# Kernel optimization log

Hardware: AMD Instinct MI355X
Metric: run time of the kernel (lower is better)

Reference implementation:

```python
import jax, jax.numpy as jnp
import numpy as np

N = 8192      # nodes
R = 3         # non-homo relations
E = 262144    # edges per relation (avg degree 32)
IN = 128      # input_dim
OUT = 64      # output_dim (= per-head dim hd)
HEAD = 4
D = OUT * HEAD  # 256, w_liner / d_liner output width


def setup_inputs() -> dict:
    key = jax.random.key(0)
    ks = jax.random.split(key, 16)
    s = 0.05  # weight scale (mimics uniform(-stdv, stdv) magnitude)
    return {
        "features": jax.random.normal(ks[0], (N, IN), jnp.float32),
        "labels_mat": jax.random.uniform(ks[1], (N, 2), jnp.float32),
        "bi_adj": jax.random.uniform(ks[2], (N, N), jnp.float32),
        "adj_mask": jax.random.uniform(ks[3], (N, N), jnp.float32),
        "Wd": jax.random.normal(ks[4], (IN, D), jnp.float32) * s,
        "bd": jax.random.normal(ks[5], (D,), jnp.float32) * s,
        "Wf": jax.random.normal(ks[6], (3 * D, 1), jnp.float32) * s,
        "bf": jax.random.normal(ks[7], (1,), jnp.float32) * s,
        "Ww": jax.random.normal(ks[8], (R, IN, D), jnp.float32) * s,
        "bw": jax.random.normal(ks[9], (R, D), jnp.float32) * s,
        "Wa": jax.random.normal(ks[10], (R, 2 * OUT), jnp.float32) * s,
        "ba": jax.random.normal(ks[11], (R,), jnp.float32) * s,
        "Wl": jax.random.normal(ks[12], (R * OUT, OUT), jnp.float32) * s,
        "bl": jax.random.normal(ks[13], (OUT,), jnp.float32) * s,
        "edges": jax.random.randint(ks[14], (R, 2, E), 0, N, jnp.int64),
    }


def reference(features, labels_mat, bi_adj, adj_mask, Wd, bd, Wf, bf,
              Ww, bw, Wa, ba, Wl, bl, edges):
    n = features.shape[0]
    r_count = edges.shape[0]
    d = Wd.shape[1]          # D = head * hd
    hd = d // HEAD

    # --- HeterophilyLearning (shared relation_aware), dropout is identity in eval.
    # score = tanh(f_liner(cat[src, dst, src-dst])); f_liner is linear, so
    # split Wf and precompute per-node contributions, then gather per edge.
    sproj = features @ Wd + bd                      # [N, D]
    w1, w2, w3 = Wf[:d, 0], Wf[d:2 * d, 0], Wf[2 * d:, 0]
    p_src = sproj @ (w1 + w3)                       # [N]
    p_dst = sproj @ (w2 - w3)                       # [N]

    hs = []
    for r in range(r_count):  # small fixed loop over relations
        src, dst = edges[r, 0], edges[r, 1]
        sign = jnp.tanh(p_src[src] + p_dst[dst] + bf[0])          # [E]
        h = (features @ Ww[r] + bw[r]).reshape(n, HEAD, hd)       # [N, H, hd]
        # atten(cat[sign*h_src, h_dst]) decomposed into src/dst node terms
        qsrc = jnp.einsum('nhd,d->nh', h, Wa[r, :hd])             # [N, H]
        qdst = jnp.einsum('nhd,d->nh', h, Wa[r, hd:])             # [N, H]
        alpha = jax.nn.leaky_relu(sign[:, None] * qsrc[src] + qdst[dst] + ba[r])  # [E, H]
        # ragged softmax over incoming edges of each dst node
        m = jax.ops.segment_max(alpha, dst, num_segments=n)
        m = jnp.where(jnp.isfinite(m), m, 0.0)
        ew = jnp.exp(alpha - m[dst])
        denom = jax.ops.segment_sum(ew, dst, num_segments=n)
        attn = ew / denom[dst]                                    # [E, H]
        sf = sign[:, None, None] * h[src]                         # [E, H, hd]
        out = jax.ops.segment_sum(attn[:, :, None] * sf, dst, num_segments=n)  # [N, H, hd]
        hs.append(out.sum(axis=1))  # if_sum=True in Aggregation -> sum heads -> [N, hd]

    hcat = jnp.concatenate(hs, axis=1)              # [N, R*hd]
    h_out = hcat @ Wl + bl                          # dropout identity in eval

    # --- Label propagation (last relation's Homo, as in the original loop)
    T = bi_adj * adj_mask
    T = T / jnp.maximum(jnp.abs(T).sum(axis=1, keepdims=True), 1e-12)  # F.normalize p=1
    y_hat = T @ labels_mat
    return h_out, y_hat
```

## Files before the change

kernel.cpp:

```cpp
#include <hip/hip_runtime.h>
#include <hip/hip_bf16.h>
#include <math.h>

constexpr int kN    = 8192;
constexpr int kR    = 3;
constexpr int kE    = 262144;
constexpr int kIn   = 128;
constexpr int kOut  = 64;
constexpr int kHead = 4;
constexpr int kD    = 256;

__global__ __launch_bounds__(256) void k_node_pre(
    const float* __restrict__ feat, const float* __restrict__ Wd,
    const float* __restrict__ bd,   const float* __restrict__ Wf,
    const float* __restrict__ Ww,   const float* __restrict__ bw,
    const float* __restrict__ Wa,
    float* __restrict__ p_src, float* __restrict__ p_dst,
    float* __restrict__ qsrc,  float* __restrict__ qdst,
    float* __restrict__ hbuf)
{
    const int n = blockIdx.x, t = threadIdx.x;
    __shared__ float f[kIn];
    __shared__ float2 red[256];

    if (t < kIn) f[t] = feat[n * kIn + t];
    __syncthreads();

    float sp = bd[t];
    #pragma unroll 8
    for (int k = 0; k < kIn; ++k) sp += f[k] * Wd[k * kD + t];

    const float w13 = Wf[t]        + Wf[2 * kD + t];
    const float w23 = Wf[kD + t]   - Wf[2 * kD + t];
    red[t] = make_float2(sp * w13, sp * w23);
    __syncthreads();
    for (int s = 128; s > 0; s >>= 1) {
        if (t < s) { red[t].x += red[t + s].x; red[t].y += red[t + s].y; }
        __syncthreads();
    }
    if (t == 0) { p_src[n] = red[0].x; p_dst[n] = red[0].y; }

    const int head = t >> 6, lane = t & 63;
    for (int r = 0; r < kR; ++r) {
        float hv = bw[r * kD + t];
        const float* W = Ww + (size_t)r * kIn * kD;
        #pragma unroll 8
        for (int k = 0; k < kIn; ++k) hv += f[k] * W[k * kD + t];
        hbuf[(size_t)r * kN * kD + (size_t)n * kD + t] = hv;

        float c1 = hv * Wa[r * 2 * kOut + lane];
        float c2 = hv * Wa[r * 2 * kOut + kOut + lane];
        for (int off = 32; off > 0; off >>= 1) {
            c1 += __shfl_down(c1, off);
            c2 += __shfl_down(c2, off);
        }
        if (lane == 0) {
            qsrc[(size_t)r * kN * kHead + n * kHead + head] = c1;
            qdst[(size_t)r * kN * kHead + n * kHead + head] = c2;
        }
    }
}

__global__ void k_hist(const int* __restrict__ dst, int* __restrict__ deg)
{
    int e = blockIdx.x * blockDim.x + threadIdx.x;
    if (e < kE) atomicAdd(&deg[dst[e]], 1);
}

__global__ __launch_bounds__(1024) void k_scan(
    const int* __restrict__ deg, int* __restrict__ rowstart)
{
    __shared__ int lds[1024];
    const int t = threadIdx.x;
    int v[8];
    int s = 0;
    #pragma unroll
    for (int k = 0; k < 8; ++k) v[k] = deg[t * 8 + k];
    #pragma unroll
    for (int k = 0; k < 8; ++k) { int tmp = s; s += v[k]; v[k] = tmp; }
    lds[t] = s;
    __syncthreads();
    for (int off = 1; off < 1024; off <<= 1) {
        int x = 0;
        if (t >= off) x = lds[t - off];
        __syncthreads();
        if (t >= off) lds[t] += x;
        __syncthreads();
    }
    const int pre = (t == 0) ? 0 : lds[t - 1];
    #pragma unroll
    for (int k = 0; k < 8; ++k) rowstart[t * 8 + k] = pre + v[k];
}

__global__ void k_scatter(
    const int* __restrict__ src_arr, const int* __restrict__ dst_arr,
    const float* __restrict__ p_src, const float* __restrict__ p_dst,
    const float* __restrict__ qsrc,  const float* __restrict__ qdst,
    const float* __restrict__ bf,    const float* __restrict__ ba, int r,
    const int* __restrict__ rowstart, int* __restrict__ cursor,
    int* __restrict__ srcs_s, float* __restrict__ sign_s,
    float4* __restrict__ alpha_s)
{
    int e = blockIdx.x * blockDim.x + threadIdx.x;
    if (e >= kE) return;
    const int s = src_arr[e], d = dst_arr[e];
    const float sg = tanhf(p_src[s] + p_dst[d] + bf[0]);
    const float bar = ba[r];
    float4 a;
    float* ap = &a.x;
    #pragma unroll
    for (int h = 0; h < kHead; ++h) {
        float x = sg * qsrc[s * kHead + h] + qdst[d * kHead + h] + bar;
        ap[h] = (x > 0.f) ? x : 0.01f * x;
    }
    const int pos = rowstart[d] + atomicAdd(&cursor[d], 1);
    srcs_s[pos] = s;
    sign_s[pos] = sg;
    alpha_s[pos] = a;
}

__global__ __launch_bounds__(256) void k_node_agg(
    const int* __restrict__ deg, const int* __restrict__ rowstart,
    const int* __restrict__ srcs_s, const float* __restrict__ sign_s,
    const float4* __restrict__ alpha_s,
    const float* __restrict__ hr,
    float* __restrict__ hcat, int r)
{
    const int n = blockIdx.x, t = threadIdx.x;
    const int dg = deg[n], start = rowstart[n];
    __shared__ float4 red4[256];
    __shared__ float lds[256];

    if (dg == 0) {
        if (t < kOut) hcat[(size_t)n * (kR * kOut) + r * kOut + t] = 0.f;
        return;
    }

    float4 mx = make_float4(-INFINITY, -INFINITY, -INFINITY, -INFINITY);
    for (int i = t; i < dg; i += 256) {
        float4 a = alpha_s[start + i];
        mx.x = fmaxf(mx.x, a.x); mx.y = fmaxf(mx.y, a.y);
        mx.z = fmaxf(mx.z, a.z); mx.w = fmaxf(mx.w, a.w);
    }
    red4[t] = mx;
    __syncthreads();
    for (int s = 128; s > 0; s >>= 1) {
        if (t < s) {
            float4 o = red4[t + s];
            red4[t].x = fmaxf(red4[t].x, o.x); red4[t].y = fmaxf(red4[t].y, o.y);
            red4[t].z = fmaxf(red4[t].z, o.z); red4[t].w = fmaxf(red4[t].w, o.w);
        }
        __syncthreads();
    }
    const float4 mm = red4[0];
    const int head = t >> 6;
    const float m_h = (head == 0) ? mm.x : (head == 1) ? mm.y : (head == 2) ? mm.z : mm.w;

    const float* af = (const float*)alpha_s;
    float acc = 0.f, dsum = 0.f;
    for (int i = 0; i < dg; ++i) {
        const int pos = start + i;
        const float sg = sign_s[pos];
        const float a  = af[(size_t)pos * 4 + head];
        const float ew = __expf(a - m_h);
        dsum += ew;
        const int s = srcs_s[pos];
        acc += ew * sg * hr[(size_t)s * kD + t];
    }
    lds[t] = acc / dsum;
    __syncthreads();
    if (t < kOut) {
        hcat[(size_t)n * (kR * kOut) + r * kOut + t] =
            lds[t] + lds[t + 64] + lds[t + 128] + lds[t + 192];
    }
}

__global__ __launch_bounds__(64) void k_hout(
    const float* __restrict__ hcat, const float* __restrict__ Wl,
    const float* __restrict__ bl, float* __restrict__ out)
{
    const int n = blockIdx.x, t = threadIdx.x;
    __shared__ float row[kR * kOut];
    for (int k = t; k < kR * kOut; k += 64) row[k] = hcat[(size_t)n * (kR * kOut) + k];
    __syncthreads();
    float acc = bl[t];
    #pragma unroll 8
    for (int k = 0; k < kR * kOut; ++k) acc += row[k] * Wl[k * kOut + t];
    out[(size_t)n * kOut + t] = acc;
}

__global__ __launch_bounds__(256) void k_yhat(
    const float* __restrict__ bi, const float* __restrict__ mask,
    const float* __restrict__ labels, float* __restrict__ out)
{
    const int n = blockIdx.x, t = threadIdx.x;
    const float4* b4 = (const float4*)(bi   + (size_t)n * kN);
    const float4* m4 = (const float4*)(mask + (size_t)n * kN);
    const float4* l4 = (const float4*)labels;
    float ss = 0.f, y0 = 0.f, y1 = 0.f;
    for (int j = t; j < kN / 4; j += 256) {
        const float4 b = b4[j], m = m4[j];
        const float4 la = l4[2 * j], lb = l4[2 * j + 1];
        const float t0 = b.x * m.x, t1 = b.y * m.y, t2 = b.z * m.z, t3 = b.w * m.w;
        ss += fabsf(t0) + fabsf(t1) + fabsf(t2) + fabsf(t3);
        y0 += t0 * la.x + t1 * la.z + t2 * lb.x + t3 * lb.z;
        y1 += t0 * la.y + t1 * la.w + t2 * lb.y + t3 * lb.w;
    }
    __shared__ float4 red[256];
    red[t] = make_float4(ss, y0, y1, 0.f);
    __syncthreads();
    for (int s = 128; s > 0; s >>= 1) {
        if (t < s) {
            red[t].x += red[t + s].x; red[t].y += red[t + s].y; red[t].z += red[t + s].z;
        }
        __syncthreads();
    }
    if (t == 0) {
        const float s = fmaxf(red[0].x, 1e-12f);
        out[(size_t)n * 2]     = red[0].y / s;
        out[(size_t)n * 2 + 1] = red[0].z / s;
    }
}

extern "C" void kernel_launch(void* const* d_in, const int* in_sizes, int n_in,
                              void* d_out, int out_size, void* d_ws, size_t ws_size,
                              hipStream_t stream)
{
    const float* feat   = (const float*)d_in[0];
    const float* labels = (const float*)d_in[1];
    const float* bi     = (const float*)d_in[2];
    const float* mask   = (const float*)d_in[3];
    const float* Wd     = (const float*)d_in[4];
    const float* bd     = (const float*)d_in[5];
    const float* Wf     = (const float*)d_in[6];
    const float* bf     = (const float*)d_in[7];
    const float* Ww     = (const float*)d_in[8];
    const float* bw     = (const float*)d_in[9];
    const float* Wa     = (const float*)d_in[10];
    const float* ba     = (const float*)d_in[11];
    const float* Wl     = (const float*)d_in[12];
    const float* bl     = (const float*)d_in[13];
    const int*   edges  = (const int*)d_in[14];
    float* out = (float*)d_out;

    float* w = (float*)d_ws;
    float* p_src  = w; w += kN;
    float* p_dst  = w; w += kN;
    float* qsrc   = w; w += (size_t)kR * kN * kHead;
    float* qdst   = w; w += (size_t)kR * kN * kHead;
    float* hbuf   = w; w += (size_t)kR * kN * kD;
    float* hcat   = w; w += (size_t)kN * kR * kOut;
    float* sign_s = w; w += kE;
    float* alpha_s= w; w += (size_t)kE * 4;
    int* srcs_s   = (int*)w; w += kE;
    int* deg      = (int*)w; w += kN;
    int* rowstart = (int*)w; w += kN;
    int* cursor   = (int*)w; w += kN;

    k_node_pre<<<kN, 256, 0, stream>>>(feat, Wd, bd, Wf, Ww, bw, Wa,
                                       p_src, p_dst, qsrc, qdst, hbuf);

    for (int r = 0; r < kR; ++r) {
        const int* src_arr = edges + (size_t)r * 2 * kE;
        const int* dst_arr = src_arr + kE;
        hipMemsetAsync(deg,    0, kN * sizeof(int), stream);
        hipMemsetAsync(cursor, 0, kN * sizeof(int), stream);
        k_hist<<<kE / 256, 256, 0, stream>>>(dst_arr, deg);
        k_scan<<<1, 1024, 0, stream>>>(deg, rowstart);
        k_scatter<<<kE / 256, 256, 0, stream>>>(
            src_arr, dst_arr, p_src, p_dst,
            qsrc + (size_t)r * kN * kHead, qdst + (size_t)r * kN * kHead,
            bf, ba, r, rowstart, cursor, srcs_s, sign_s, (float4*)alpha_s);
        k_node_agg<<<kN, 256, 0, stream>>>(
            deg, rowstart, srcs_s, sign_s, (const float4*)alpha_s,
            hbuf + (size_t)r * kN * kD, hcat, r);
    }

    k_hout<<<kN, 64, 0, stream>>>(hcat, Wl, bl, out);
    k_yhat<<<kN, 256, 0, stream>>>(bi, mask, labels, out + (size_t)kN * kOut);
}
```

Baseline: 989.2 us.

## Fold projection weights, batch node GEMM, merge relation launches, stage edges in LDS

Adds a prep kernel that folds Wd·Wf and Ww·Wa into small column vectors, so p_src/p_dst and qsrc/qdst become direct dot products with the features. The node pre-pass now computes 16 nodes per block to reuse each Ww load across nodes. The per-relation loop of hist/scan/scatter/agg is collapsed into single launches using a relation grid dimension. The aggregation kernel caches up to 128 edges' alpha/sign/src in LDS. This removes the redundant sproj GEMM and many small launches, at the cost of more workspace and a serial single-block prep kernel.

```diff
diff --git a/kernel.cpp b/kernel.cpp
--- a/kernel.cpp
+++ b/kernel.cpp
@@ -9,67 +9,133 @@
 constexpr int kOut  = 64;
 constexpr int kHead = 4;
 constexpr int kD    = 256;
+constexpr int NB    = 16;
+constexpr int kCols = 2 + 2 * kR * kHead;
+
+__global__ __launch_bounds__(256) void k_prep(
+    const float* __restrict__ Wd, const float* __restrict__ bd,
+    const float* __restrict__ Wf, const float* __restrict__ Ww,
+    const float* __restrict__ bw, const float* __restrict__ Wa,
+    float* __restrict__ V, float* __restrict__ C)
+{
+    const int t = threadIdx.x;
+    for (int task = t; task < kCols * kIn; task += 256) {
+        const int row = task >> 7;
+        const int k   = task & 127;
+        float s = 0.f;
+        if (row < 2) {
+            for (int c = 0; c < kD; ++c) {
+                const float w = (row == 0) ? (Wf[c] + Wf[2 * kD + c])
+                                           : (Wf[kD + c] - Wf[2 * kD + c]);
+                s += Wd[k * kD + c] * w;
+            }
+        } else {
+            const int idx = row - 2;
+            const int src = idx < kR * kHead;
+            const int rel = (src ? idx : idx - kR * kHead) >> 2;
+            const int h   = (src ? idx : idx - kR * kHead) & 3;
+            const float* wwk = Ww + ((size_t)rel * kIn + k) * kD + h * kOut;
+            const float* wa  = Wa + rel * 2 * kOut + (src ? 0 : kOut);
+            for (int d = 0; d < kOut; ++d) s += wwk[d] * wa[d];
+        }
+        V[row * kIn + k] = s;
+    }
+    if (t < kCols) {
+        const int row = t;
+        float s = 0.f;
+        if (row < 2) {
+            for (int c = 0; c < kD; ++c) {
+                const float w = (row == 0) ? (Wf[c] + Wf[2 * kD + c])
+                                           : (Wf[kD + c] - Wf[2 * kD + c]);
+                s += bd[c] * w;
+            }
+        } else {
+            const int idx = row - 2;
+            const int src = idx < kR * kHead;
+            const int rel = (src ? idx : idx - kR * kHead) >> 2;
+            const int h   = (src ? idx : idx - kR * kHead) & 3;
+            const float* bwr = bw + rel * kD + h * kOut;
+            const float* wa  = Wa + rel * 2 * kOut + (src ? 0 : kOut);
+            for (int d = 0; d < kOut; ++d) s += bwr[d] * wa[d];
+        }
+        C[row] = s;
+    }
+}
 
 __global__ __launch_bounds__(256) void k_node_pre(
-    const float* __restrict__ feat, const float* __restrict__ Wd,
-    const float* __restrict__ bd,   const float* __restrict__ Wf,
-    const float* __restrict__ Ww,   const float* __restrict__ bw,
-    const float* __restrict__ Wa,
-    float* __restrict__ p_src, float* __restrict__ p_dst,
-    float* __restrict__ qsrc,  float* __restrict__ qdst,
-    float* __restrict__ hbuf)
-{
-    const int n = blockIdx.x, t = threadIdx.x;
-    __shared__ float f[kIn];
-    __shared__ float2 red[256];
-
-    if (t < kIn) f[t] = feat[n * kIn + t];
-    __syncthreads();
-
-    float sp = bd[t];
-    #pragma unroll 8
-    for (int k = 0; k < kIn; ++k) sp += f[k] * Wd[k * kD + t];
-
-    const float w13 = Wf[t]        + Wf[2 * kD + t];
-    const float w23 = Wf[kD + t]   - Wf[2 * kD + t];
-    red[t] = make_float2(sp * w13, sp * w23);
-    __syncthreads();
-    for (int s = 128; s > 0; s >>= 1) {
-        if (t < s) { red[t].x += red[t + s].x; red[t].y += red[t + s].y; }
-        __syncthreads();
-    }
-    if (t == 0) { p_src[n] = red[0].x; p_dst[n] = red[0].y; }
-
-    const int head = t >> 6, lane = t & 63;
+    const float* __restrict__ feat, const float* __restrict__ Ww,
+    const float* __restrict__ bw,   const float* __restrict__ V,
+    const float* __restrict__ C,
+    float* __restrict__ hbuf, float* __restrict__ p_src, float* __restrict__ p_dst,
+    float* __restrict__ qsrc, float* __restrict__ qdst)
+{
+    const int nb = blockIdx.x * NB;
+    const int t  = threadIdx.x;
+    __shared__ float f[NB][kIn];
+
+    const float4* fg = (const float4*)(feat + (size_t)nb * kIn);
+    float4* fl = (float4*)f;
+    for (int i = t; i < NB * kIn / 4; i += 256) fl[i] = fg[i];
+    __syncthreads();
+
     for (int r = 0; r < kR; ++r) {
-        float hv = bw[r * kD + t];
         const float* W = Ww + (size_t)r * kIn * kD;
-        #pragma unroll 8
-        for (int k = 0; k < kIn; ++k) hv += f[k] * W[k * kD + t];
-        hbuf[(size_t)r * kN * kD + (size_t)n * kD + t] = hv;
-
-        float c1 = hv * Wa[r * 2 * kOut + lane];
-        float c2 = hv * Wa[r * 2 * kOut + kOut + lane];
-        for (int off = 32; off > 0; off >>= 1) {
-            c1 += __shfl_down(c1, off);
-            c2 += __shfl_down(c2, off);
-        }
-        if (lane == 0) {
-            qsrc[(size_t)r * kN * kHead + n * kHead + head] = c1;
-            qdst[(size_t)r * kN * kHead + n * kHead + head] = c2;
-        }
-    }
-}
-
-__global__ void k_hist(const int* __restrict__ dst, int* __restrict__ deg)
-{
-    int e = blockIdx.x * blockDim.x + threadIdx.x;
-    if (e < kE) atomicAdd(&deg[dst[e]], 1);
+        const float b = bw[r * kD + t];
+        float acc[NB];
+        #pragma unroll
+        for (int j = 0; j < NB; ++j) acc[j] = b;
+        for (int k4 = 0; k4 < kIn / 4; ++k4) {
+            const float w0 = W[(k4 * 4 + 0) * kD + t];
+            const float w1 = W[(k4 * 4 + 1) * kD + t];
+            const float w2 = W[(k4 * 4 + 2) * kD + t];
+            const float w3 = W[(k4 * 4 + 3) * kD + t];
+            #pragma unroll
+            for (int j = 0; j < NB; ++j) {
+                const float4 fv = *(const float4*)&f[j][k4 * 4];
+                acc[j] += fv.x * w0 + fv.y * w1 + fv.z * w2 + fv.w * w3;
+            }
+        }
+        float* hb = hbuf + ((size_t)r * kN + nb) * kD + t;
+        #pragma unroll
+        for (int j = 0; j < NB; ++j) hb[(size_t)j * kD] = acc[j];
+    }
+
+    for (int task = t; task < NB * kCols; task += 256) {
+        const int j = task / kCols, col = task % kCols;
+        const float* v = V + col * kIn;
+        float s = C[col];
+        for (int k4 = 0; k4 < kIn / 4; ++k4) {
+            const float4 fv = *(const float4*)&f[j][k4 * 4];
+            const float4 vv = *(const float4*)&v[k4 * 4];
+            s += fv.x * vv.x + fv.y * vv.y + fv.z * vv.z + fv.w * vv.w;
+        }
+        const int n = nb + j;
+        if (col == 0)      p_src[n] = s;
+        else if (col == 1) p_dst[n] = s;
+        else if (col < 2 + kR * kHead) {
+            const int idx = col - 2;
+            qsrc[((size_t)(idx >> 2) * kN + n) * kHead + (idx & 3)] = s;
+        } else {
+            const int idx = col - 2 - kR * kHead;
+            qdst[((size_t)(idx >> 2) * kN + n) * kHead + (idx & 3)] = s;
+        }
+    }
+}
+
+__global__ void k_hist(const int* __restrict__ edges, int* __restrict__ deg)
+{
+    const int r = blockIdx.y;
+    const int e = blockIdx.x * blockDim.x + threadIdx.x;
+    const int d = edges[(size_t)r * 2 * kE + kE + e];
+    atomicAdd(&deg[r * kN + d], 1);
 }
 
 __global__ __launch_bounds__(1024) void k_scan(
-    const int* __restrict__ deg, int* __restrict__ rowstart)
-{
+    const int* __restrict__ deg_all, int* __restrict__ rowstart_all)
+{
+    const int r = blockIdx.x;
+    const int* deg = deg_all + r * kN;
+    int* rowstart = rowstart_all + r * kN;
     __shared__ int lds[1024];
     const int t = threadIdx.x;
     int v[8];
@@ -93,43 +159,57 @@
 }
 
 __global__ void k_scatter(
-    const int* __restrict__ src_arr, const int* __restrict__ dst_arr,
+    const int* __restrict__ edges,
     const float* __restrict__ p_src, const float* __restrict__ p_dst,
-    const float* __restrict__ qsrc,  const float* __restrict__ qdst,
-    const float* __restrict__ bf,    const float* __restrict__ ba, int r,
+    const float* __restrict__ qsrc_all, const float* __restrict__ qdst_all,
+    const float* __restrict__ bf, const float* __restrict__ ba,
     const int* __restrict__ rowstart, int* __restrict__ cursor,
     int* __restrict__ srcs_s, float* __restrict__ sign_s,
     float4* __restrict__ alpha_s)
 {
-    int e = blockIdx.x * blockDim.x + threadIdx.x;
-    if (e >= kE) return;
-    const int s = src_arr[e], d = dst_arr[e];
+    const int r = blockIdx.y;
+    const int e = blockIdx.x * blockDim.x + threadIdx.x;
+    const int s = edges[(size_t)r * 2 * kE + e];
+    const int d = edges[(size_t)r * 2 * kE + kE + e];
     const float sg = tanhf(p_src[s] + p_dst[d] + bf[0]);
     const float bar = ba[r];
+    const float4 qs = *(const float4*)&qsrc_all[((size_t)r * kN + s) * kHead];
+    const float4 qd = *(const float4*)&qdst_all[((size_t)r * kN + d) * kHead];
     float4 a;
-    float* ap = &a.x;
-    #pragma unroll
-    for (int h = 0; h < kHead; ++h) {
-        float x = sg * qsrc[s * kHead + h] + qdst[d * kHead + h] + bar;
-        ap[h] = (x > 0.f) ? x : 0.01f * x;
-    }
-    const int pos = rowstart[d] + atomicAdd(&cursor[d], 1);
-    srcs_s[pos] = s;
-    sign_s[pos] = sg;
-    alpha_s[pos] = a;
+    a.x = sg * qs.x + qd.x + bar;
+    a.y = sg * qs.y + qd.y + bar;
+    a.z = sg * qs.z + qd.z + bar;
+    a.w = sg * qs.w + qd.w + bar;
+    a.x = (a.x > 0.f) ? a.x : 0.01f * a.x;
+    a.y = (a.y > 0.f) ? a.y : 0.01f * a.y;
+    a.z = (a.z > 0.f) ? a.z : 0.01f * a.z;
+    a.w = (a.w > 0.f) ? a.w : 0.01f * a.w;
+    const int pos = rowstart[r * kN + d] + atomicAdd(&cursor[r * kN + d], 1);
+    srcs_s[(size_t)r * kE + pos] = s;
+    sign_s[(size_t)r * kE + pos] = sg;
+    alpha_s[(size_t)r * kE + pos] = a;
 }
 
 __global__ __launch_bounds__(256) void k_node_agg(
     const int* __restrict__ deg, const int* __restrict__ rowstart,
-    const int* __restrict__ srcs_s, const float* __restrict__ sign_s,
-    const float4* __restrict__ alpha_s,
-    const float* __restrict__ hr,
-    float* __restrict__ hcat, int r)
-{
+    const int* __restrict__ srcs_all, const float* __restrict__ sign_all,
+    const float4* __restrict__ alpha_all, const float* __restrict__ hbuf,
+    float* __restrict__ hcat)
+{
+    const int r = blockIdx.y;
     const int n = blockIdx.x, t = threadIdx.x;
-    const int dg = deg[n], start = rowstart[n];
+    const int dg = deg[r * kN + n], start = rowstart[r * kN + n];
+    const float* hr = hbuf + (size_t)r * kN * kD;
+    const int* srcs = srcs_all + (size_t)r * kE;
+    const float* sgn = sign_all + (size_t)r * kE;
+    const float4* al = alpha_all + (size_t)r * kE;
+
+    constexpr int CAP = 128;
     __shared__ float4 red4[256];
-    __shared__ float lds[256];
+    __shared__ float4 s_al[CAP];
+    __shared__ float  s_sg[CAP];
+    __shared__ int    s_sr[CAP];
+    __shared__ float  lds[256];
 
     if (dg == 0) {
         if (t < kOut) hcat[(size_t)n * (kR * kOut) + r * kOut + t] = 0.f;
@@ -138,7 +218,12 @@
 
     float4 mx = make_float4(-INFINITY, -INFINITY, -INFINITY, -INFINITY);
     for (int i = t; i < dg; i += 256) {
-        float4 a = alpha_s[start + i];
+        const float4 a = al[start + i];
+        if (i < CAP) {
+            s_al[i] = a;
+            s_sg[i] = sgn[start + i];
+            s_sr[i] = srcs[start + i];
+        }
         mx.x = fmaxf(mx.x, a.x); mx.y = fmaxf(mx.y, a.y);
         mx.z = fmaxf(mx.z, a.z); mx.w = fmaxf(mx.w, a.w);
     }
@@ -146,7 +231,7 @@
     __syncthreads();
     for (int s = 128; s > 0; s >>= 1) {
         if (t < s) {
-            float4 o = red4[t + s];
+            const float4 o = red4[t + s];
             red4[t].x = fmaxf(red4[t].x, o.x); red4[t].y = fmaxf(red4[t].y, o.y);
             red4[t].z = fmaxf(red4[t].z, o.z); red4[t].w = fmaxf(red4[t].w, o.w);
         }
@@ -154,18 +239,23 @@
     }
     const float4 mm = red4[0];
     const int head = t >> 6;
-    const float m_h = (head == 0) ? mm.x : (head == 1) ? mm.y : (head == 2) ? mm.z : mm.w;
-
-    const float* af = (const float*)alpha_s;
+    const float m_h = (head == 0) ? mm.x : (head == 1) ? mm.y
+                    : (head == 2) ? mm.z : mm.w;
+
     float acc = 0.f, dsum = 0.f;
-    for (int i = 0; i < dg; ++i) {
-        const int pos = start + i;
-        const float sg = sign_s[pos];
-        const float a  = af[(size_t)pos * 4 + head];
+    const int m = (dg < CAP) ? dg : CAP;
+    for (int i = 0; i < m; ++i) {
+        const float a  = ((const float*)&s_al[i])[head];
         const float ew = __expf(a - m_h);
         dsum += ew;
-        const int s = srcs_s[pos];
-        acc += ew * sg * hr[(size_t)s * kD + t];
+        acc += ew * s_sg[i] * hr[(size_t)s_sr[i] * kD + t];
+    }
+    for (int i = CAP; i < dg; ++i) {
+        const int pos = start + i;
+        const float a  = ((const float*)&al[pos])[head];
+        const float ew = __expf(a - m_h);
+        dsum += ew;
+        acc += ew * sgn[pos] * hr[(size_t)srcs[pos] * kD + t];
     }
     lds[t] = acc / dsum;
     __syncthreads();
@@ -248,33 +338,29 @@
     float* p_dst  = w; w += kN;
     float* qsrc   = w; w += (size_t)kR * kN * kHead;
     float* qdst   = w; w += (size_t)kR * kN * kHead;
+    float* V      = w; w += kCols * kIn;
+    float* C      = w; w += 32;
     float* hbuf   = w; w += (size_t)kR * kN * kD;
     float* hcat   = w; w += (size_t)kN * kR * kOut;
-    float* sign_s = w; w += kE;
-    float* alpha_s= w; w += (size_t)kE * 4;
-    int* srcs_s   = (int*)w; w += kE;
-    int* deg      = (int*)w; w += kN;
-    int* rowstart = (int*)w; w += kN;
-    int* cursor   = (int*)w; w += kN;
-
-    k_node_pre<<<kN, 256, 0, stream>>>(feat, Wd, bd, Wf, Ww, bw, Wa,
-                                       p_src, p_dst, qsrc, qdst, hbuf);
-
-    for (int r = 0; r < kR; ++r) {
-        const int* src_arr = edges + (size_t)r * 2 * kE;
-        const int* dst_arr = src_arr + kE;
-        hipMemsetAsync(deg,    0, kN * sizeof(int), stream);
-        hipMemsetAsync(cursor, 0, kN * sizeof(int), stream);
-        k_hist<<<kE / 256, 256, 0, stream>>>(dst_arr, deg);
-        k_scan<<<1, 1024, 0, stream>>>(deg, rowstart);
-        k_scatter<<<kE / 256, 256, 0, stream>>>(
-            src_arr, dst_arr, p_src, p_dst,
-            qsrc + (size_t)r * kN * kHead, qdst + (size_t)r * kN * kHead,
-            bf, ba, r, rowstart, cursor, srcs_s, sign_s, (float4*)alpha_s);
-        k_node_agg<<<kN, 256, 0, stream>>>(
-            deg, rowstart, srcs_s, sign_s, (const float4*)alpha_s,
-            hbuf + (size_t)r * kN * kD, hcat, r);
-    }
+    float* sign_s = w; w += (size_t)kR * kE;
+    float* alpha_s= w; w += (size_t)kR * kE * 4;
+    int* srcs_s   = (int*)w; w += (size_t)kR * kE;
+    int* deg      = (int*)w; w += kR * kN;
+    int* cursor   = (int*)w; w += kR * kN;
+    int* rowstart = (int*)w; w += kR * kN;
+
+    k_prep<<<1, 256, 0, stream>>>(Wd, bd, Wf, Ww, bw, Wa, V, C);
+    k_node_pre<<<kN / NB, 256, 0, stream>>>(feat, Ww, bw, V, C,
+                                            hbuf, p_src, p_dst, qsrc, qdst);
+
+    hipMemsetAsync(deg, 0, 2 * kR * kN * sizeof(int), stream);
+    k_hist<<<dim3(kE / 256, kR), 256, 0, stream>>>(edges, deg);
+    k_scan<<<kR, 1024, 0, stream>>>(deg, rowstart);
+    k_scatter<<<dim3(kE / 256, kR), 256, 0, stream>>>(
+        edges, p_src, p_dst, qsrc, qdst, bf, ba,
+        rowstart, cursor, srcs_s, sign_s, (float4*)alpha_s);
+    k_node_agg<<<dim3(kN, kR), 256, 0, stream>>>(
+        deg, rowstart, srcs_s, sign_s, (const float4*)alpha_s, hbuf, hcat);
 
     k_hout<<<kN, 64, 0, stream>>>(hcat, Wl, bl, out);
     k_yhat<<<kN, 256, 0, stream>>>(bi, mask, labels, out + (size_t)kN * kOut);
```

Result: faster. 870.3 us (-12.0%).
